# Kernel optimization log

Measured on AMD Instinct MI355X. Metric: run time of the kernel, lower is better.

The kernel has to match this reference:

```python
import jax, jax.numpy as jnp
import numpy as np

B, S = 8, 2500
E, F = 128, 128          # embed_size, num_filter_maps
L = 8921                 # num_classes
V = 50002                # vocab_size + 2
KERNELS = (3, 5, 9)


def _conv1d_same(x, w, b):
    # x: [B, C_in, S], w: [C_out, C_in, K], b: [C_out]; 'same' padding for odd K
    k = w.shape[-1]
    pad = k // 2
    out = jax.lax.conv_general_dilated(
        x, w, window_strides=(1,), padding=[(pad, pad)],
        dimension_numbers=('NCH', 'OIH', 'NCH'))
    return out + b[None, :, None]


def setup_inputs() -> dict:
    key = jax.random.key(0)
    ks = jax.random.split(key, 12)
    inp = {
        'docs': jax.random.randint(ks[0], (B, S), 0, 50000),
        'doc_masks': jnp.ones((B, S), dtype=jnp.float32),
        'doc_lengths': jax.random.randint(ks[1], (B,), 1, S),
        'leaf_idxs': jnp.arange(L),
        'embed_w': jax.random.normal(ks[2], (V, E), dtype=jnp.float32) * 0.02,
        'word_U_w': jax.random.normal(ks[3], (L, F), dtype=jnp.float32) * 0.05,
        'final_w': jax.random.normal(ks[4], (L, F), dtype=jnp.float32) * 0.05,
        'final_b': jnp.zeros((L,), dtype=jnp.float32),
    }
    for i, k in enumerate(KERNELS):
        scale = (2.0 / (E * k)) ** 0.5
        inp[f'conv_w{k}'] = jax.random.normal(ks[5 + i], (F, E, k), dtype=jnp.float32) * scale
        inp[f'conv_b{k}'] = jnp.zeros((F,), dtype=jnp.float32)
    return inp


def reference(docs, doc_masks, doc_lengths, leaf_idxs, embed_w, word_U_w,
              final_w, final_b, conv_w3, conv_b3, conv_w5, conv_b5,
              conv_w9, conv_b9):
    # embed + transpose -> [B, E, S]  (dropout is identity at eval)
    x = embed_w[docs].transpose(0, 2, 1)
    # multi-kernel conv1d + tanh, stack, elementwise max -> [B, F, S]
    feats = jnp.stack([
        jnp.tanh(_conv1d_same(x, conv_w3, conv_b3)),
        jnp.tanh(_conv1d_same(x, conv_w5, conv_b5)),
        jnp.tanh(_conv1d_same(x, conv_w9, conv_b9)),
    ], axis=1)
    word_features = jnp.max(feats, axis=1)  # [B, F, S]
    # CAML label attention
    wu = word_U_w[leaf_idxs]                                   # [L, F]
    alpha = jax.nn.softmax(jnp.einsum('lf,bfs->bls', wu, word_features), axis=2)
    context = jnp.einsum('bls,bfs->blf', alpha, word_features)  # [B, L, F]
    y = jnp.einsum('blf,lf->bl', context, final_w) + final_b    # [B, L]
    return (y, context)
```

## Files before the change

kernel.cpp:

```cpp
#include <hip/hip_runtime.h>
#include <hip/hip_bf16.h>

#define BB 8
#define SS 2500
#define EE 128
#define FF 128
#define LL 8921

using bf8 = __attribute__((ext_vector_type(8))) short;
using bf4 = __attribute__((ext_vector_type(4))) short;
using f4  = __attribute__((ext_vector_type(4))) float;

__device__ __forceinline__ short f2bf(float f) {
  unsigned u = __builtin_bit_cast(unsigned, f);
  u += 0x7fffu + ((u >> 16) & 1u);
  return (short)(u >> 16);
}

__device__ __forceinline__ void gll16(const void* g, void* l) {
  __builtin_amdgcn_global_load_lds(
      (const __attribute__((address_space(1))) unsigned int*)g,
      (__attribute__((address_space(3))) unsigned int*)l, 16, 0, 0);
}

template <int CTRL>
__device__ __forceinline__ float dppmv(float x) {
  int r = __builtin_amdgcn_update_dpp(0, __builtin_bit_cast(int, x), CTRL, 0xF, 0xF, false);
  return __builtin_bit_cast(float, r);
}
__device__ __forceinline__ float rowsum16(float x) {
  x += dppmv<0xB1>(x);
  x += dppmv<0x4E>(x);
  x += dppmv<0x124>(x);
  x += dppmv<0x128>(x);
  return x;
}

__global__ void prep_kernel(const int* __restrict__ docs, const int* __restrict__ leaf,
                            const float* __restrict__ embed, const float* __restrict__ wu,
                            const float* __restrict__ w3, const float* __restrict__ w5,
                            const float* __restrict__ w9,
                            short* __restrict__ x_bf, short* __restrict__ wu_bf,
                            short* __restrict__ wpack) {
  const int NX = BB * SS * EE / 8;
  const int NU = LL * FF / 8;
  const int NW = 17 * FF * EE;
  int tid = blockIdx.x * 256 + threadIdx.x;
  if (tid < NX) {
    int base = tid * 8;
    int bs = base >> 7, e0 = base & 127;
    int row = docs[bs];
    const float* p = embed + (row << 7) + e0;
    bf8 o;
#pragma unroll
    for (int i = 0; i < 8; ++i) o[i] = f2bf(p[i]);
    *(bf8*)(x_bf + base) = o;
  } else if (tid < NX + NU) {
    int base = (tid - NX) * 8;
    int l = base >> 7, f0 = base & 127;
    int row = leaf[l];
    const float* p = wu + (row << 7) + f0;
    bf8 o;
#pragma unroll
    for (int i = 0; i < 8; ++i) o[i] = f2bf(p[i]);
    *(bf8*)(wu_bf + base) = o;
  } else if (tid < NX + NU + NW) {
    int i = tid - NX - NU;
    int t = i >> 14, fe = i & 16383;
    const float* w; int K, dk;
    if (t < 3)      { w = w3; K = 3; dk = t; }
    else if (t < 8) { w = w5; K = 5; dk = t - 3; }
    else            { w = w9; K = 9; dk = t - 8; }
    wpack[i] = f2bf(w[fe * K + dk]);
  }
}

__global__ __launch_bounds__(256, 2) void conv_kernel(
    const short* __restrict__ x_bf, const short* __restrict__ wpack,
    const float* __restrict__ cb3, const float* __restrict__ cb5, const float* __restrict__ cb9,
    short* __restrict__ wf, short* __restrict__ wfT) {
  __shared__ short xt[72][136];
  __shared__ short wt[128][136];
  int b = blockIdx.x;
  int s0 = blockIdx.y * 64;
  int tid = threadIdx.x, wid = tid >> 6, lane = tid & 63, g = lane >> 4, c = lane & 15;

  for (int i = tid; i < 72 * 16; i += 256) {
    int r = i >> 4, c8 = (i & 15) << 3, s = s0 + r - 4;
    bf8 v = {0, 0, 0, 0, 0, 0, 0, 0};
    if (s >= 0 && s < SS) v = *(const bf8*)(x_bf + ((b * SS + s) << 7) + c8);
    *(bf8*)&xt[r][c8] = v;
  }

  bf8 wpre[8];
#pragma unroll
  for (int k = 0; k < 8; ++k) {
    int i = tid + (k << 8); int r = i >> 4, c8 = (i & 15) << 3;
    wpre[k] = *(const bf8*)(wpack + (r << 7) + c8);
  }

  float wfm[8][4];
#pragma unroll
  for (int j = 0; j < 8; ++j)
#pragma unroll
    for (int i = 0; i < 4; ++i) wfm[j][i] = -1e30f;

  int tap = 0;
  for (int kid = 0; kid < 3; ++kid) {
    const float* cb = (kid == 0) ? cb3 : (kid == 1) ? cb5 : cb9;
    const int K = (kid == 0) ? 3 : (kid == 1) ? 5 : 9;
    const int pad = K >> 1;
    f4 acc[8];
#pragma unroll
    for (int j = 0; j < 8; ++j) {
      float bvj = cb[j * 16 + c];
      acc[j] = (f4){bvj, bvj, bvj, bvj};
    }
    for (int dk = 0; dk < K; ++dk, ++tap) {
      __syncthreads();
#pragma unroll
      for (int k = 0; k < 8; ++k) {
        int i = tid + (k << 8); int r = i >> 4, c8 = (i & 15) << 3;
        *(bf8*)&wt[r][c8] = wpre[k];
      }
      if (tap < 16) {
#pragma unroll
        for (int k = 0; k < 8; ++k) {
          int i = tid + (k << 8); int r = i >> 4, c8 = (i & 15) << 3;
          wpre[k] = *(const bf8*)(wpack + (tap + 1) * 16384 + (r << 7) + c8);
        }
      }
      __syncthreads();
      int xr = wid * 16 + c + dk - pad + 4;
      __builtin_amdgcn_s_setprio(1);
#pragma unroll
      for (int ks = 0; ks < 4; ++ks) {
        bf8 a = *(const bf8*)&xt[xr][ks * 32 + g * 8];
#pragma unroll
        for (int j = 0; j < 8; ++j) {
          bf8 bb = *(const bf8*)&wt[j * 16 + c][ks * 32 + g * 8];
          acc[j] = __builtin_amdgcn_mfma_f32_16x16x32_bf16(a, bb, acc[j], 0, 0, 0);
        }
      }
      __builtin_amdgcn_s_setprio(0);
    }
#pragma unroll
    for (int j = 0; j < 8; ++j)
#pragma unroll
      for (int i = 0; i < 4; ++i) wfm[j][i] = fmaxf(wfm[j][i], tanhf(acc[j][i]));
  }

  int sb = s0 + wid * 16 + g * 4;
#pragma unroll
  for (int j = 0; j < 8; ++j) {
    int f = j * 16 + c;
#pragma unroll
    for (int i = 0; i < 4; ++i) {
      int s = sb + i;
      if (s < SS) wf[((b * SS + s) << 7) + f] = f2bf(wfm[j][i]);
    }
    int tbase = (b * 128 + f) * SS + sb;
    if (sb + 3 < SS) {
      bf4 pk;
#pragma unroll
      for (int i = 0; i < 4; ++i) pk[i] = f2bf(wfm[j][i]);
      *(bf4*)(wfT + tbase) = pk;
    } else {
#pragma unroll
      for (int i = 0; i < 4; ++i)
        if (sb + i < SS) wfT[tbase + i] = f2bf(wfm[j][i]);
    }
  }
}

__global__ __launch_bounds__(256, 3) void attn_kernel(
    const short* __restrict__ wu_bf, const short* __restrict__ wf, const short* __restrict__ wfT,
    float* __restrict__ ctx) {
  __shared__ short kt[64 * 128];
  __shared__ short vt[128 * 64];
  __shared__ short pt[128][68];
  int b = blockIdx.x;
  int l0 = blockIdx.y * 128;
  int tid = threadIdx.x, wid = tid >> 6, lane = tid & 63, g = lane >> 4, c = lane & 15;

  int k_row[4], k_off[4], v_off[4];
#pragma unroll
  for (int k = 0; k < 4; ++k) {
    int idx = (k * 4 + wid) * 64 + lane;
    int r = idx >> 4, ck = idx & 15;
    k_row[k] = r;
    k_off[k] = (ck ^ (r & 15)) << 3;
    int rv = idx >> 3, cv = idx & 7;
    v_off[k] = (b * 128 + rv) * SS + ((cv ^ (rv & 7)) << 3);
  }
  const short* wfb = wf + b * SS * 128;

  bf8 q[2][4];
#pragma unroll
  for (int ms = 0; ms < 2; ++ms) {
    int l = l0 + wid * 32 + ms * 16 + c;
    if (l >= LL) l = LL - 1;
#pragma unroll
    for (int ks = 0; ks < 4; ++ks)
      q[ms][ks] = *(const bf8*)(wu_bf + (l << 7) + ks * 32 + g * 8);
  }

  float lst[2][4];
  f4 o[2][8];
#pragma unroll
  for (int ms = 0; ms < 2; ++ms) {
#pragma unroll
    for (int i = 0; i < 4; ++i) lst[ms][i] = 0.0f;
#pragma unroll
    for (int n = 0; n < 8; ++n) o[ms][n] = (f4){0.f, 0.f, 0.f, 0.f};
  }

  for (int t = 0; t < 40; ++t) {
    int s0 = t * 64;
    bool full = (s0 + 64 <= SS);
    __syncthreads();
#pragma unroll
    for (int k = 0; k < 4; ++k) {
      int s = s0 + k_row[k];
      if (s > SS - 1) s = SS - 1;
      gll16(wfb + s * 128 + k_off[k], (char*)kt + (k * 4 + wid) * 1024);
    }
    if (full) {
#pragma unroll
      for (int k = 0; k < 4; ++k)
        gll16(wfT + v_off[k] + s0, (char*)vt + (k * 4 + wid) * 1024);
    } else {
      for (int idx = tid; idx < 128 * 64; idx += 256) {
        int r = idx >> 6, sl = idx & 63, so = s0 + sl;
        short v = (so < SS) ? wfT[(b * 128 + r) * SS + so] : (short)0;
        vt[(r << 6) + (((sl >> 3) ^ (r & 7)) << 3) + (sl & 7)] = v;
      }
    }
    __syncthreads();

    float rs[2][4] = {{0.f, 0.f, 0.f, 0.f}, {0.f, 0.f, 0.f, 0.f}};
#pragma unroll
    for (int jh = 0; jh < 2; ++jh) {
      f4 sc[2][2];
#pragma unroll
      for (int ms = 0; ms < 2; ++ms)
#pragma unroll
        for (int jj = 0; jj < 2; ++jj) sc[ms][jj] = (f4){0.f, 0.f, 0.f, 0.f};
      __builtin_amdgcn_s_setprio(1);
#pragma unroll
      for (int ks = 0; ks < 4; ++ks) {
        int xk = (((ks << 2) | g) ^ c) << 3;
        bf8 kb[2];
#pragma unroll
        for (int jj = 0; jj < 2; ++jj)
          kb[jj] = *(const bf8*)&kt[((jh * 2 + jj) * 16 + c) * 128 + xk];
#pragma unroll
        for (int ms = 0; ms < 2; ++ms)
#pragma unroll
          for (int jj = 0; jj < 2; ++jj)
            sc[ms][jj] = __builtin_amdgcn_mfma_f32_16x16x32_bf16(q[ms][ks], kb[jj], sc[ms][jj], 0, 0, 0);
      }
      __builtin_amdgcn_s_setprio(0);
#pragma unroll
      for (int jj = 0; jj < 2; ++jj) {
        int j = jh * 2 + jj;
        int col = j * 16 + c;
        bool masked = (!full) && (s0 + col >= SS);
#pragma unroll
        for (int ms = 0; ms < 2; ++ms) {
          int rbase = wid * 32 + ms * 16 + g * 4;
#pragma unroll
          for (int i = 0; i < 4; ++i) {
            float p = masked ? 0.0f : __expf(sc[ms][jj][i]);
            pt[rbase + i][col] = f2bf(p);
            rs[ms][i] += p;
          }
        }
      }
    }
#pragma unroll
    for (int ms = 0; ms < 2; ++ms)
#pragma unroll
      for (int i = 0; i < 4; ++i) lst[ms][i] += rowsum16(rs[ms][i]);
    asm volatile("s_waitcnt lgkmcnt(0)" ::: "memory");
    __builtin_amdgcn_sched_barrier(0);

    __builtin_amdgcn_s_setprio(1);
#pragma unroll
    for (int ks = 0; ks < 2; ++ks) {
      bf8 pa[2];
#pragma unroll
      for (int ms = 0; ms < 2; ++ms) {
        const short* pp = &pt[wid * 32 + ms * 16 + c][ks * 32 + g * 8];
        bf4 lo = *(const bf4*)pp; bf4 hi = *(const bf4*)(pp + 4);
        pa[ms] = __builtin_shufflevector(lo, hi, 0, 1, 2, 3, 4, 5, 6, 7);
      }
      int xv = (((ks << 2) | g) ^ (c & 7)) << 3;
#pragma unroll
      for (int n = 0; n < 8; ++n) {
        bf8 vb = *(const bf8*)&vt[(n * 16 + c) * 64 + xv];
#pragma unroll
        for (int ms = 0; ms < 2; ++ms)
          o[ms][n] = __builtin_amdgcn_mfma_f32_16x16x32_bf16(pa[ms], vb, o[ms][n], 0, 0, 0);
      }
    }
    __builtin_amdgcn_s_setprio(0);
  }

#pragma unroll
  for (int ms = 0; ms < 2; ++ms)
#pragma unroll
    for (int i = 0; i < 4; ++i) {
      int l = l0 + wid * 32 + ms * 16 + g * 4 + i;
      if (l < LL) {
        float inv = 1.0f / lst[ms][i];
        int rb = (b * LL + l) << 7;
#pragma unroll
        for (int n = 0; n < 8; ++n) ctx[rb + n * 16 + c] = o[ms][n][i] * inv;
      }
    }
}

__global__ void y_kernel(const float* __restrict__ ctx, const float* __restrict__ fw,
                         const float* __restrict__ fb, float* __restrict__ y) {
  int wid = threadIdx.x >> 6, lane = threadIdx.x & 63;
  int row = blockIdx.x * 4 + wid;
  if (row >= BB * LL) return;
  int l = row % LL;
  const float* cp = ctx + (row << 7);
  const float* wp = fw + (l << 7);
  float s = cp[lane] * wp[lane] + cp[lane + 64] * wp[lane + 64];
#pragma unroll
  for (int d = 32; d >= 1; d >>= 1) s += __shfl_xor(s, d);
  if (lane == 0) y[row] = s + fb[l];
}

extern "C" void kernel_launch(void* const* d_in, const int* in_sizes, int n_in,
                              void* d_out, int out_size, void* d_ws, size_t ws_size,
                              hipStream_t stream) {
  const int* docs = (const int*)d_in[0];
  const int* leaf = (const int*)d_in[3];
  const float* embed = (const float*)d_in[4];
  const float* wu = (const float*)d_in[5];
  const float* fw = (const float*)d_in[6];
  const float* fb = (const float*)d_in[7];
  const float* w3 = (const float*)d_in[8];
  const float* b3 = (const float*)d_in[9];
  const float* w5 = (const float*)d_in[10];
  const float* b5 = (const float*)d_in[11];
  const float* w9 = (const float*)d_in[12];
  const float* b9 = (const float*)d_in[13];

  char* ws = (char*)d_ws;
  short* x_bf  = (short*)(ws);
  short* wu_bf = (short*)(ws + 5120000);
  short* wpack = (short*)(ws + 7403776);
  short* wfp   = (short*)(ws + 7960832);
  short* wfT   = (short*)(ws + 13080832);

  float* y = (float*)d_out;
  float* ctx = (float*)d_out + BB * LL;

  prep_kernel<<<2896, 256, 0, stream>>>(docs, leaf, embed, wu, w3, w5, w9, x_bf, wu_bf, wpack);
  conv_kernel<<<dim3(8, 40), 256, 0, stream>>>(x_bf, wpack, b3, b5, b9, wfp, wfT);
  attn_kernel<<<dim3(8, 70), 256, 0, stream>>>(wu_bf, wfp, wfT, ctx);
  y_kernel<<<(BB * LL) / 4, 256, 0, stream>>>(ctx, fw, fb, y);
}
```

Measured before the change: 217.2 us.

## Fuse final projection into attention kernel, use exp2 with prescaled queries, split barriers

The final label projection (y) is now computed in the attention epilogue from the in-register context values, so the separate y_kernel launch and its re-read of ctx are gone. Query weights are prescaled by log2(e) during prep so the softmax can use exp2f instead of __expf. The __syncthreads calls are replaced with explicit barriers plus vmcnt/lgkmcnt waits, so the QK^T compute can start while the V-tile loads are still in flight. The hand-placed wait counts must match the number of outstanding loads, and an extra barrier is added before the PV stage.

```diff
diff --git a/kernel.cpp b/kernel.cpp
--- a/kernel.cpp
+++ b/kernel.cpp
@@ -62,7 +62,7 @@
     const float* p = wu + (row << 7) + f0;
     bf8 o;
 #pragma unroll
-    for (int i = 0; i < 8; ++i) o[i] = f2bf(p[i]);
+    for (int i = 0; i < 8; ++i) o[i] = f2bf(p[i] * 1.4426950408889634f);
     *(bf8*)(wu_bf + base) = o;
   } else if (tid < NX + NU + NW) {
     int i = tid - NX - NU;
@@ -175,7 +175,8 @@
 
 __global__ __launch_bounds__(256, 3) void attn_kernel(
     const short* __restrict__ wu_bf, const short* __restrict__ wf, const short* __restrict__ wfT,
-    float* __restrict__ ctx) {
+    const float* __restrict__ fw, const float* __restrict__ fb,
+    float* __restrict__ y, float* __restrict__ ctx) {
   __shared__ short kt[64 * 128];
   __shared__ short vt[128 * 64];
   __shared__ short pt[128][68];
@@ -218,7 +219,9 @@
   for (int t = 0; t < 40; ++t) {
     int s0 = t * 64;
     bool full = (s0 + 64 <= SS);
-    __syncthreads();
+    asm volatile("s_waitcnt lgkmcnt(0)" ::: "memory");
+    __builtin_amdgcn_s_barrier();
+    __builtin_amdgcn_sched_barrier(0);
 #pragma unroll
     for (int k = 0; k < 4; ++k) {
       int s = s0 + k_row[k];
@@ -235,8 +238,11 @@
         short v = (so < SS) ? wfT[(b * 128 + r) * SS + so] : (short)0;
         vt[(r << 6) + (((sl >> 3) ^ (r & 7)) << 3) + (sl & 7)] = v;
       }
-    }
-    __syncthreads();
+      asm volatile("s_waitcnt lgkmcnt(0)" ::: "memory");
+    }
+    asm volatile("s_waitcnt vmcnt(4)" ::: "memory");
+    __builtin_amdgcn_s_barrier();
+    __builtin_amdgcn_sched_barrier(0);
 
     float rs[2][4] = {{0.f, 0.f, 0.f, 0.f}, {0.f, 0.f, 0.f, 0.f}};
 #pragma unroll
@@ -271,7 +277,7 @@
           int rbase = wid * 32 + ms * 16 + g * 4;
 #pragma unroll
           for (int i = 0; i < 4; ++i) {
-            float p = masked ? 0.0f : __expf(sc[ms][jj][i]);
+            float p = masked ? 0.0f : exp2f(sc[ms][jj][i]);
             pt[rbase + i][col] = f2bf(p);
             rs[ms][i] += p;
           }
@@ -282,6 +288,10 @@
     for (int ms = 0; ms < 2; ++ms)
 #pragma unroll
       for (int i = 0; i < 4; ++i) lst[ms][i] += rowsum16(rs[ms][i]);
+
+    asm volatile("s_waitcnt vmcnt(0)" ::: "memory");
+    __builtin_amdgcn_s_barrier();
+    __builtin_amdgcn_sched_barrier(0);
     asm volatile("s_waitcnt lgkmcnt(0)" ::: "memory");
     __builtin_amdgcn_sched_barrier(0);
 
@@ -315,24 +325,17 @@
       if (l < LL) {
         float inv = 1.0f / lst[ms][i];
         int rb = (b * LL + l) << 7;
-#pragma unroll
-        for (int n = 0; n < 8; ++n) ctx[rb + n * 16 + c] = o[ms][n][i] * inv;
-      }
-    }
-}
-
-__global__ void y_kernel(const float* __restrict__ ctx, const float* __restrict__ fw,
-                         const float* __restrict__ fb, float* __restrict__ y) {
-  int wid = threadIdx.x >> 6, lane = threadIdx.x & 63;
-  int row = blockIdx.x * 4 + wid;
-  if (row >= BB * LL) return;
-  int l = row % LL;
-  const float* cp = ctx + (row << 7);
-  const float* wp = fw + (l << 7);
-  float s = cp[lane] * wp[lane] + cp[lane + 64] * wp[lane + 64];
-#pragma unroll
-  for (int d = 32; d >= 1; d >>= 1) s += __shfl_xor(s, d);
-  if (lane == 0) y[row] = s + fb[l];
+        float acc = 0.0f;
+#pragma unroll
+        for (int n = 0; n < 8; ++n) {
+          float cv = o[ms][n][i] * inv;
+          ctx[rb + n * 16 + c] = cv;
+          acc += cv * fw[(l << 7) + n * 16 + c];
+        }
+        acc = rowsum16(acc);
+        if (c == 0) y[b * LL + l] = acc + fb[l];
+      }
+    }
 }
 
 extern "C" void kernel_launch(void* const* d_in, const int* in_sizes, int n_in,
@@ -363,6 +366,5 @@
 
   prep_kernel<<<2896, 256, 0, stream>>>(docs, leaf, embed, wu, w3, w5, w9, x_bf, wu_bf, wpack);
   conv_kernel<<<dim3(8, 40), 256, 0, stream>>>(x_bf, wpack, b3, b5, b9, wfp, wfT);
-  attn_kernel<<<dim3(8, 70), 256, 0, stream>>>(wu_bf, wfp, wfT, ctx);
-  y_kernel<<<(BB * LL) / 4, 256, 0, stream>>>(ctx, fw, fb, y);
-}
+  attn_kernel<<<dim3(8, 70), 256, 0, stream>>>(wu_bf, wfp, wfT, fw, fb, y, ctx);
+}
```

Measured after the change: 226.2 us. +4.2%, slower.
